# Performance work log

Measured on AMD Instinct MI355X. Metric: run time of the kernel, lower is better.

Reference implementation:

```python
import jax, jax.numpy as jnp
import numpy as np

N_NODES = 100000
EPS = 1e-5


def gcn_conv(x, edge_index, W, b):
    # PyG GCNConv: add self loops, symmetric normalization, aggregate at target.
    n = x.shape[0]
    xw = x @ W                                  # [N, F_out]
    loop = jnp.arange(n)
    src = jnp.concatenate([edge_index[0], loop])
    dst = jnp.concatenate([edge_index[1], loop])
    deg = jax.ops.segment_sum(jnp.ones_like(dst, dtype=xw.dtype), dst, num_segments=n)
    dinv = jnp.where(deg > 0, jax.lax.rsqrt(deg), 0.0)
    norm = dinv[src] * dinv[dst]                # [E+N]
    out = jax.ops.segment_sum(norm[:, None] * xw[src], dst, num_segments=n)
    return out + b


def batch_norm(x, gamma, beta):
    # training-mode BatchNorm1d over node dim
    m = x.mean(axis=0)
    v = x.var(axis=0)
    return (x - m) * jax.lax.rsqrt(v + EPS) * gamma + beta


def setup_inputs() -> dict:
    key = jax.random.key(0)
    ks = jax.random.split(key, 16)
    dims = [(128, 256), (256, 128), (128, 64)]
    inp = {
        "x": jax.random.normal(ks[0], (N_NODES, 128), dtype=jnp.float32),
        "edge_index": jax.random.randint(ks[1], (2, 1600000), 0, N_NODES),
        "pos_edge_index": jax.random.randint(ks[2], (2, 200000), 0, N_NODES),
        "neg_edge_index": jax.random.randint(ks[3], (2, 200000), 0, N_NODES),
    }
    for i, (fi, fo) in enumerate(dims, start=1):
        inp[f"W{i}"] = jax.random.normal(ks[3 + i], (fi, fo), dtype=jnp.float32) / np.sqrt(fi)
        inp[f"b{i}"] = jnp.zeros((fo,), dtype=jnp.float32)
        inp[f"g{i}"] = jnp.ones((fo,), dtype=jnp.float32)
        inp[f"beta{i}"] = jnp.zeros((fo,), dtype=jnp.float32)
    return inp


def reference(x, edge_index, pos_edge_index, neg_edge_index,
              W1, b1, g1, beta1, W2, b2, g2, beta2, W3, b3, g3, beta3):
    # encode
    h = gcn_conv(x, edge_index, W1, b1)
    h = jax.nn.sigmoid(batch_norm(h, g1, beta1))
    h = gcn_conv(h, edge_index, W2, b2)
    h = jax.nn.sigmoid(batch_norm(h, g2, beta2))
    h = gcn_conv(h, edge_index, W3, b3)
    z = batch_norm(h, g3, beta3)                # [N, 64]
    # decode
    ei = jnp.concatenate([pos_edge_index, neg_edge_index], axis=-1)
    logits = jnp.sum(z[ei[0]] * z[ei[1]], axis=-1)
    return logits
```

## Files before the change

### kernel.cpp

```cpp
#include <hip/hip_runtime.h>
#include <hip/hip_bf16.h>
#include <stddef.h>


#define WAVE 64
#define BSHIFT 9
#define SCHUNK 4096

typedef __attribute__((ext_vector_type(8))) short short8;
typedef __attribute__((ext_vector_type(4))) float f32x4;

__device__ __forceinline__ float bl(uint g) { return __uint_as_float(g << 16); }
__device__ __forceinline__ float bh(uint g) { return __uint_as_float(g & 0xffff0000u); }
__device__ __forceinline__ ushort f2b(float f) {
    uint u = __float_as_uint(f);
    return (ushort)((u + 0x7fffu + ((u >> 16) & 1u)) >> 16);
}
__device__ __forceinline__ uint pack2(float lo, float hi) {
    return (uint)f2b(lo) | ((uint)f2b(hi) << 16);
}

__device__ __forceinline__ void gload16(const ushort* g, ushort* l) {
    __builtin_amdgcn_global_load_lds(
        (const __attribute__((address_space(1))) uint*)g,
        (__attribute__((address_space(3))) uint*)l, 16, 0, 0);
}

__global__ __launch_bounds__(256) void k_bhist(const int* __restrict__ dst, int* __restrict__ gh, int E) {
    __shared__ int lh[256];
    lh[threadIdx.x] = 0; __syncthreads();
    int i = blockIdx.x * 256 + threadIdx.x, stride = gridDim.x * 256;
    for (; i < E; i += stride) atomicAdd(&lh[dst[i] >> BSHIFT], 1);
    __syncthreads();
    int v = lh[threadIdx.x];
    if (v) atomicAdd(&gh[threadIdx.x], v);
}

__global__ void k_bscan(const int* __restrict__ gh, int* __restrict__ boff, int* __restrict__ bcur) {
    __shared__ int ls[256];
    int t = threadIdx.x;
    int v = gh[t];
    ls[t] = v; __syncthreads();
    for (int off = 1; off < 256; off <<= 1) {
        int x = (t >= off) ? ls[t - off] : 0;
        __syncthreads();
        ls[t] += x;
        __syncthreads();
    }
    int excl = ls[t] - v;
    boff[t] = excl; bcur[t] = excl;
    if (t == 255) boff[256] = ls[255];
}

__global__ __launch_bounds__(256) void k_bscatter(const int* __restrict__ src, const int* __restrict__ dst,
                                                  int* __restrict__ gcur, uint* __restrict__ pairs, int E) {
    __shared__ int lh[256];
    int t = threadIdx.x;
    int base = blockIdx.x * SCHUNK;
    lh[t] = 0; __syncthreads();
    int rs[16], rd[16];
    #pragma unroll
    for (int i = 0; i < 16; ++i) {
        int idx = base + i * 256 + t;
        if (idx < E) { rs[i] = src[idx]; rd[i] = dst[idx]; atomicAdd(&lh[rd[i] >> BSHIFT], 1); }
        else rd[i] = -1;
    }
    __syncthreads();
    int cnt_b = lh[t];
    int b0 = cnt_b ? atomicAdd(&gcur[t], cnt_b) : 0;
    lh[t] = b0;
    __syncthreads();
    #pragma unroll
    for (int i = 0; i < 16; ++i) {
        if (rd[i] >= 0) {
            int p = atomicAdd(&lh[rd[i] >> BSHIFT], 1);
            pairs[p] = ((uint)(rd[i] & 511) << 17) | (uint)rs[i];
        }
    }
}

__global__ __launch_bounds__(256) void k_bfine(const uint* __restrict__ pairs, const int* __restrict__ boff,
                                               int* __restrict__ rowptr, int* __restrict__ srcs,
                                               float* __restrict__ dinv, int N, int E) {
    __shared__ int lcnt[512];
    __shared__ int ls[256];
    int b = blockIdx.x, t = threadIdx.x;
    int d0 = b << BSHIFT;
    int e0 = boff[b], e1 = boff[b + 1];
    lcnt[t] = 0; lcnt[t + 256] = 0;
    __syncthreads();
    for (int e = e0 + t; e < e1; e += 256)
        atomicAdd(&lcnt[pairs[e] >> 17], 1);
    __syncthreads();
    int c0 = lcnt[2 * t], c1 = lcnt[2 * t + 1];
    ls[t] = c0 + c1;
    __syncthreads();
    for (int off = 1; off < 256; off <<= 1) {
        int x = (t >= off) ? ls[t - off] : 0;
        __syncthreads();
        ls[t] += x;
        __syncthreads();
    }
    int excl = ls[t] - (c0 + c1);
    int s0 = excl, s1 = excl + c0;
    int d = d0 + 2 * t;
    if (d < N)     { rowptr[d] = e0 + s0;     dinv[d] = rsqrtf((float)(c0 + 1)); }
    if (d + 1 < N) { rowptr[d + 1] = e0 + s1; dinv[d + 1] = rsqrtf((float)(c1 + 1)); }
    if (b == 0 && t == 0) rowptr[N] = E;
    lcnt[2 * t] = s0; lcnt[2 * t + 1] = s1;
    __syncthreads();
    for (int e = e0 + t; e < e1; e += 256) {
        uint p = pairs[e];
        int pos = atomicAdd(&lcnt[p >> 17], 1);
        srcs[e0 + pos] = (int)(p & 0x1FFFFu);
    }
}

__global__ void k_conv(const float* __restrict__ W1, const float* __restrict__ W2,
                       const float* __restrict__ W3, ushort* __restrict__ Wt1,
                       ushort* __restrict__ Wt2, ushort* __restrict__ Wt3,
                       const float* __restrict__ x, const float* __restrict__ dinv,
                       ushort* __restrict__ xs, size_t n4) {
    size_t i = (size_t)blockIdx.x * 256 + threadIdx.x;
    if (i < 73728) {
        const float* W; ushort* Wt; int K, Nn; size_t j;
        if (i < 32768)      { W = W1; Wt = Wt1; K = 128; Nn = 256; j = i; }
        else if (i < 65536) { W = W2; Wt = Wt2; K = 256; Nn = 128; j = i - 32768; }
        else                { W = W3; Wt = Wt3; K = 128; Nn = 64;  j = i - 65536; }
        int k = (int)(j / Nn), n = (int)(j % Nn);
        Wt[(size_t)n * K + k] = f2b(W[(size_t)k * Nn + n]);
        return;
    }
    size_t j = i - 73728;
    if (j >= n4) return;
    float d = dinv[j / 32];
    float4 v = reinterpret_cast<const float4*>(x)[j];
    uint2 o;
    o.x = pack2(d * v.x, d * v.y);
    o.y = pack2(d * v.z, d * v.w);
    reinterpret_cast<uint2*>(xs)[j] = o;
}

template<int F, bool STATS>
__global__ __launch_bounds__(256) void k_agg(const ushort* __restrict__ in, ushort* __restrict__ out,
                                             const int* __restrict__ rowptr, const int* __restrict__ srcs,
                                             const float* __restrict__ dinv, int N,
                                             float* __restrict__ gsum, float* __restrict__ gsq) {
    constexpr int L = (F * 2) / 16;
    int wv = threadIdx.x >> 6, lane = threadIdx.x & 63;
    int node = (blockIdx.x * 4 + wv) * (64 / L) + lane / L;
    int sl = lane % L;
    bool act = node < N;
    const uint4* inq = reinterpret_cast<const uint4*>(in);
    float o[8] = {0.f, 0.f, 0.f, 0.f, 0.f, 0.f, 0.f, 0.f};
    if (act) {
        float di = dinv[node];
        float acc[8];
        {
            uint4 v = inq[(size_t)node * L + sl];
            acc[0] = bl(v.x); acc[1] = bh(v.x);
            acc[2] = bl(v.y); acc[3] = bh(v.y);
            acc[4] = bl(v.z); acc[5] = bh(v.z);
            acc[6] = bl(v.w); acc[7] = bh(v.w);
        }
        int e = rowptr[node], e1 = rowptr[node + 1];
        for (; e + 7 < e1; e += 8) {
            int s[8];
            #pragma unroll
            for (int i = 0; i < 8; ++i) s[i] = srcs[e + i];
            uint4 v[8];
            #pragma unroll
            for (int i = 0; i < 8; ++i) v[i] = inq[(size_t)s[i] * L + sl];
            #pragma unroll
            for (int i = 0; i < 8; ++i) {
                acc[0] += bl(v[i].x); acc[1] += bh(v[i].x);
                acc[2] += bl(v[i].y); acc[3] += bh(v[i].y);
                acc[4] += bl(v[i].z); acc[5] += bh(v[i].z);
                acc[6] += bl(v[i].w); acc[7] += bh(v[i].w);
            }
        }
        for (; e + 3 < e1; e += 4) {
            int s[4];
            #pragma unroll
            for (int i = 0; i < 4; ++i) s[i] = srcs[e + i];
            uint4 v[4];
            #pragma unroll
            for (int i = 0; i < 4; ++i) v[i] = inq[(size_t)s[i] * L + sl];
            #pragma unroll
            for (int i = 0; i < 4; ++i) {
                acc[0] += bl(v[i].x); acc[1] += bh(v[i].x);
                acc[2] += bl(v[i].y); acc[3] += bh(v[i].y);
                acc[4] += bl(v[i].z); acc[5] += bh(v[i].z);
                acc[6] += bl(v[i].w); acc[7] += bh(v[i].w);
            }
        }
        for (; e < e1; ++e) {
            uint4 v0 = inq[(size_t)srcs[e] * L + sl];
            acc[0] += bl(v0.x); acc[1] += bh(v0.x);
            acc[2] += bl(v0.y); acc[3] += bh(v0.y);
            acc[4] += bl(v0.z); acc[5] += bh(v0.z);
            acc[6] += bl(v0.w); acc[7] += bh(v0.w);
        }
        #pragma unroll
        for (int j = 0; j < 8; ++j) o[j] = acc[j] * di;
        uint4 ov;
        ov.x = pack2(o[0], o[1]); ov.y = pack2(o[2], o[3]);
        ov.z = pack2(o[4], o[5]); ov.w = pack2(o[6], o[7]);
        reinterpret_cast<uint4*>(out)[(size_t)node * L + sl] = ov;
    }
    if constexpr (STATS) {
        __shared__ float lsum[4][L][8], lsq[4][L][8];
        float s[8], q[8];
        #pragma unroll
        for (int j = 0; j < 8; ++j) { s[j] = o[j]; q[j] = o[j] * o[j]; }
        #pragma unroll
        for (int m = L; m < 64; m <<= 1) {
            #pragma unroll
            for (int j = 0; j < 8; ++j) { s[j] += __shfl_xor(s[j], m); q[j] += __shfl_xor(q[j], m); }
        }
        if (lane < L) {
            #pragma unroll
            for (int j = 0; j < 8; ++j) { lsum[wv][lane][j] = s[j]; lsq[wv][lane][j] = q[j]; }
        }
        __syncthreads();
        int t = threadIdx.x;
        if (t < F) {
            int ch = t / 8, j = t % 8;
            float S = 0.f, Q = 0.f;
            #pragma unroll
            for (int w = 0; w < 4; ++w) { S += lsum[w][ch][j]; Q += lsq[w][ch][j]; }
            atomicAdd(&gsum[t], S); atomicAdd(&gsq[t], Q);
        }
    }
}

template<int K, int NF, int NPASS, bool STATS, bool PRESCALE, bool APPLY>
__global__ __launch_bounds__(256) void k_gemm(const ushort* __restrict__ A, const ushort* __restrict__ Wt,
                                              ushort* __restrict__ C, int M, int Nout,
                                              const float* __restrict__ dinv,
                                              float* __restrict__ gsum, float* __restrict__ gsq,
                                              const float* __restrict__ bsum, const float* __restrict__ bsq,
                                              const float* __restrict__ bg, const float* __restrict__ bb,
                                              float invN) {
    constexpr int S = K / 64;
    constexpr int KS = K / 32;
    __shared__ ushort Alds[2][128 * 64];
    int m0 = blockIdx.x * 128;
    int t = threadIdx.x;
    int w = t >> 6, lane = t & 63;
    int wr = w >> 1, wc = w & 1;
    int rf = lane & 15, kg = lane >> 4;

    auto stage = [&](int buf, int step) {
        #pragma unroll
        for (int i = 0; i < 4; ++i) {
            int cb = (i * 4 + w) * 64;
            int chunk = cb + lane;
            int r = chunk >> 3, cs = chunk & 7;
            int c = cs ^ (r & 7);
            int gr = m0 + r; if (gr >= M) gr = M - 1;
            gload16(A + (size_t)gr * K + step * 64 + c * 8, &Alds[buf][cb * 8]);
        }
    };

    int cg_ = (t & 7) ^ ((t >> 3) & 7);
    auto stageA = [&](int buf, int s) {
        float sc[8], sh[8];
        int fb = s * 64 + cg_ * 8;
        #pragma unroll
        for (int j = 0; j < 8; ++j) {
            float m = bsum[fb + j] * invN;
            float var = bsq[fb + j] * invN - m * m;
            float sv = bg[fb + j] * rsqrtf(var + 1e-5f);
            sc[j] = sv; sh[j] = bb[fb + j] - m * sv;
        }
        #pragma unroll
        for (int i = 0; i < 4; ++i) {
            int r = (t >> 3) + i * 32;
            int gr = m0 + r; if (gr >= M) gr = M - 1;
            uint4 v = *reinterpret_cast<const uint4*>(A + (size_t)gr * K + s * 64 + cg_ * 8);
            uint u[4] = {v.x, v.y, v.z, v.w};
            #pragma unroll
            for (int j = 0; j < 4; ++j) {
                float x0 = bl(u[j]) * sc[2 * j] + sh[2 * j];
                float x1 = bh(u[j]) * sc[2 * j + 1] + sh[2 * j + 1];
                x0 = 1.f / (1.f + __expf(-x0));
                x1 = 1.f / (1.f + __expf(-x1));
                u[j] = pack2(x0, x1);
            }
            v.x = u[0]; v.y = u[1]; v.z = u[2]; v.w = u[3];
            *reinterpret_cast<uint4*>(&Alds[buf][(size_t)(r * 8 + (t & 7)) * 8]) = v;
        }
    };

    auto do_stage = [&](int buf, int step) {
        if constexpr (APPLY) stageA(buf, step); else stage(buf, step);
    };

    float dreg[4][4];
    if constexpr (PRESCALE) {
        #pragma unroll
        for (int mf = 0; mf < 4; ++mf)
            #pragma unroll
            for (int j = 0; j < 4; ++j) {
                int row = m0 + wr * 64 + mf * 16 + kg * 4 + j;
                dreg[mf][j] = (row < M) ? dinv[row] : 0.f;
            }
    }

    for (int pass = 0; pass < NPASS; ++pass) {
        int n0 = pass * NF * 32;
        const ushort* bp[NF];
        #pragma unroll
        for (int nf = 0; nf < NF; ++nf)
            bp[nf] = Wt + (size_t)(n0 + wc * (NF * 16) + nf * 16 + rf) * K + kg * 8;

        f32x4 acc[4][NF];
        #pragma unroll
        for (int mf = 0; mf < 4; ++mf)
            #pragma unroll
            for (int nf = 0; nf < NF; ++nf)
                acc[mf][nf] = (f32x4){0.f, 0.f, 0.f, 0.f};

        if (pass == 0) {
            do_stage(0, 0);
            if constexpr (S == 2) do_stage(1, 1);
            __syncthreads();
        }

        short8 bcur[NF];
        #pragma unroll
        for (int nf = 0; nf < NF; ++nf)
            bcur[nf] = *reinterpret_cast<const short8*>(bp[nf]);

        for (int s = 0; s < S; ++s) {
            if constexpr (S > 2) {
                if (s + 1 < S && pass == 0) do_stage((s + 1) & 1, s + 1);
            }
            #pragma unroll
            for (int ksl = 0; ksl < 2; ++ksl) {
                int gs = s * 2 + ksl;
                short8 bnxt[NF];
                if (gs + 1 < KS) {
                    #pragma unroll
                    for (int nf = 0; nf < NF; ++nf)
                        bnxt[nf] = *reinterpret_cast<const short8*>(bp[nf] + (gs + 1) * 32);
                }
                short8 a[4];
                #pragma unroll
                for (int mf = 0; mf < 4; ++mf) {
                    int R = wr * 64 + mf * 16 + rf;
                    int idx = R * 8 + ((ksl * 4 + kg) ^ (R & 7));
                    a[mf] = *reinterpret_cast<const short8*>(&Alds[s & 1][idx * 8]);
                }
                #pragma unroll
                for (int mf = 0; mf < 4; ++mf)
                    #pragma unroll
                    for (int nf = 0; nf < NF; ++nf)
                        acc[mf][nf] = __builtin_amdgcn_mfma_f32_16x16x32_bf16(a[mf], bcur[nf], acc[mf][nf], 0, 0, 0);
                if (gs + 1 < KS) {
                    #pragma unroll
                    for (int nf = 0; nf < NF; ++nf) bcur[nf] = bnxt[nf];
                }
            }
            if constexpr (S > 2) __syncthreads();
        }

        #pragma unroll
        for (int mf = 0; mf < 4; ++mf)
            #pragma unroll
            for (int nf = 0; nf < NF; ++nf) {
                int col = n0 + wc * (NF * 16) + nf * 16 + rf;
                #pragma unroll
                for (int j = 0; j < 4; ++j) {
                    int row = m0 + wr * 64 + mf * 16 + kg * 4 + j;
                    float v = acc[mf][nf][j];
                    if constexpr (PRESCALE) v *= dreg[mf][j];
                    if (row < M) C[(size_t)row * Nout + col] = f2b(v);
                }
            }

        if constexpr (STATS) {
            __shared__ float bns[2][NF * 32], bnq[2][NF * 32];
            __syncthreads();
            #pragma unroll
            for (int nf = 0; nf < NF; ++nf) {
                float cs = 0.f, cq = 0.f;
                #pragma unroll
                for (int mf = 0; mf < 4; ++mf)
                    #pragma unroll
                    for (int j = 0; j < 4; ++j) {
                        int row = m0 + wr * 64 + mf * 16 + kg * 4 + j;
                        float v = (row < M) ? acc[mf][nf][j] : 0.f;
                        cs += v; cq += v * v;
                    }
                cs += __shfl_xor(cs, 16); cs += __shfl_xor(cs, 32);
                cq += __shfl_xor(cq, 16); cq += __shfl_xor(cq, 32);
                if (kg == 0) { bns[wr][wc * (NF * 16) + nf * 16 + rf] = cs; bnq[wr][wc * (NF * 16) + nf * 16 + rf] = cq; }
            }
            __syncthreads();
            if (t < NF * 32) {
                atomicAdd(&gsum[n0 + t], bns[0][t] + bns[1][t]);
                atomicAdd(&gsq[n0 + t],  bnq[0][t] + bnq[1][t]);
            }
        }
    }
}

__global__ __launch_bounds__(256) void k_decode(const ushort* __restrict__ h,
                                                const float* __restrict__ bsum, const float* __restrict__ bsq,
                                                const float* __restrict__ bg, const float* __restrict__ bb,
                                                float invN,
                                                const int* __restrict__ pos, const int* __restrict__ neg,
                                                int Pp, int Pn, float* __restrict__ out) {
    __shared__ float scl[64], shl[64];
    int t = threadIdx.x;
    if (t < 64) {
        float m = bsum[t] * invN;
        float var = bsq[t] * invN - m * m;
        float sc = bg[t] * rsqrtf(var + 1e-5f);
        scl[t] = sc; shl[t] = bb[t] - m * sc;
    }
    __syncthreads();
    int gid = blockIdx.x * 16 + (t >> 4);
    int l = t & 15;
    int P = Pp + Pn;
    if (gid >= P) return;
    int a, b;
    if (gid < Pp) { a = pos[gid]; b = pos[Pp + gid]; }
    else          { int e = gid - Pp; a = neg[e]; b = neg[Pn + e]; }
    const uint2* hu = reinterpret_cast<const uint2*>(h);
    uint2 ua = hu[(size_t)a * 16 + l];
    uint2 ub = hu[(size_t)b * 16 + l];
    int f = l * 4;
    float s0 = scl[f], s1 = scl[f + 1], s2 = scl[f + 2], s3 = scl[f + 3];
    float t0 = shl[f], t1 = shl[f + 1], t2 = shl[f + 2], t3 = shl[f + 3];
    float a0 = bl(ua.x) * s0 + t0, a1 = bh(ua.x) * s1 + t1, a2 = bl(ua.y) * s2 + t2, a3 = bh(ua.y) * s3 + t3;
    float b0 = bl(ub.x) * s0 + t0, b1 = bh(ub.x) * s1 + t1, b2 = bl(ub.y) * s2 + t2, b3 = bh(ub.y) * s3 + t3;
    float d = a0 * b0 + a1 * b1 + a2 * b2 + a3 * b3;
    d += __shfl_xor(d, 1);
    d += __shfl_xor(d, 2);
    d += __shfl_xor(d, 4);
    d += __shfl_xor(d, 8);
    if (l == 0) out[gid] = d;
}

extern "C" void kernel_launch(void* const* d_in, const int* in_sizes, int n_in,
                              void* d_out, int out_size, void* d_ws, size_t ws_size,
                              hipStream_t stream) {
    const float* x   = (const float*)d_in[0];
    const int*   ei  = (const int*)d_in[1];
    const int*   pe  = (const int*)d_in[2];
    const int*   ne  = (const int*)d_in[3];
    const float* W1  = (const float*)d_in[4];
    const float* g1  = (const float*)d_in[6];
    const float* be1 = (const float*)d_in[7];
    const float* W2  = (const float*)d_in[8];
    const float* g2  = (const float*)d_in[10];
    const float* be2 = (const float*)d_in[11];
    const float* W3  = (const float*)d_in[12];
    const float* g3  = (const float*)d_in[14];
    const float* be3 = (const float*)d_in[15];
    float* out = (float*)d_out;

    const int N  = in_sizes[0] / 128;
    const int E  = in_sizes[1] / 2;
    const int Pp = in_sizes[2] / 2;
    const int Pn = in_sizes[3] / 2;
    const float invN = 1.0f / (float)N;

    char* ws = (char*)d_ws;
    auto carve = [&](size_t bytes) -> char* {
        char* p = ws;
        ws += (bytes + 255) & ~(size_t)255;
        return p;
    };
    char*  zz     = carve(256 * 4 + 896 * 4);
    int*   gh     = (int*)zz;
    float* sums1  = (float*)(zz + 1024);
    float* sq1    = sums1 + 256;
    float* sums2  = sq1 + 256;
    float* sq2    = sums2 + 128;
    float* sums3  = sq2 + 128;
    float* sq3    = sums3 + 64;
    size_t zz_bytes = 1024 + 896 * 4;

    int*    boff   = (int*)carve(257 * 4);
    int*    bcur   = (int*)carve(256 * 4);
    int*    rowptr = (int*)carve((size_t)(N + 1) * 4);
    float*  dinv   = (float*)carve((size_t)N * 4);
    int*    srcs   = (int*)carve((size_t)E * 4);
    uint*   pairs  = (uint*)carve((size_t)E * 4);
    ushort* Wt1    = (ushort*)carve(128 * 256 * 2);
    ushort* Wt2    = (ushort*)carve(256 * 128 * 2);
    ushort* Wt3    = (ushort*)carve(128 * 64 * 2);
    ushort* b1     = (ushort*)carve((size_t)N * 128 * 2);
    ushort* b2     = (ushort*)carve((size_t)N * 128 * 2);
    ushort* b3     = (ushort*)carve((size_t)N * 256 * 2);

    const int* e_src = ei;
    const int* e_dst = ei + E;
    const int NBUCK = (N + (1 << BSHIFT) - 1) >> BSHIFT;

    hipMemsetAsync(zz, 0, zz_bytes, stream);

    k_bhist<<<2048, 256, 0, stream>>>(e_dst, gh, E);
    k_bscan<<<1, 256, 0, stream>>>(gh, boff, bcur);
    k_bscatter<<<(E + SCHUNK - 1) / SCHUNK, 256, 0, stream>>>(e_src, e_dst, bcur, pairs, E);
    k_bfine<<<NBUCK, 256, 0, stream>>>(pairs, boff, rowptr, srcs, dinv, N, E);

    {
        size_t n4 = (size_t)N * 128 / 4;
        int blocks = (int)((73728 + n4 + 255) / 256);
        k_conv<<<blocks, 256, 0, stream>>>(W1, W2, W3, Wt1, Wt2, Wt3, x, dinv, b1, n4);
    }

    const int mblk = (N + 127) / 128;
    const int agg128 = (N + 15) / 16;
    const int agg64  = (N + 31) / 32;

    k_agg<128, false><<<agg128, 256, 0, stream>>>(b1, b2, rowptr, srcs, dinv, N, nullptr, nullptr);
    k_gemm<128, 4, 2, true, false, false><<<mblk, 256, 0, stream>>>(
        b2, Wt1, b3, N, 256, nullptr, sums1, sq1, nullptr, nullptr, nullptr, nullptr, invN);

    k_gemm<256, 4, 1, false, true, true><<<mblk, 256, 0, stream>>>(
        b3, Wt2, b1, N, 128, dinv, nullptr, nullptr, sums1, sq1, g1, be1, invN);
    k_agg<128, true><<<agg128, 256, 0, stream>>>(b1, b2, rowptr, srcs, dinv, N, sums2, sq2);

    k_gemm<128, 2, 1, false, true, true><<<mblk, 256, 0, stream>>>(
        b2, Wt3, b1, N, 64, dinv, nullptr, nullptr, sums2, sq2, g2, be2, invN);
    k_agg<64, true><<<agg64, 256, 0, stream>>>(b1, b2, rowptr, srcs, dinv, N, sums3, sq3);

    k_decode<<<(Pp + Pn + 15) / 16, 256, 0, stream>>>(b2, sums3, sq3, g3, be3, invN,
                                                      pe, ne, Pp, Pn, out);
}
```

Before: 658.0 us.

## Merge preprocessing kernels, drop dinv prescale of x, split BN stats from aggregation

Fuses the destination histogram, weight transpose/convert, and x-to-bf16 conversion into one launch, so the x conversion no longer waits on the CSR build for dinv. The first aggregation now applies the source dinv per edge through an extra gather. BatchNorm statistics move out of the aggregation kernels into a separate grid-strided reduction kernel, which removes the shared-memory reduction and atomics from the aggregation. In exchange it adds launches, re-reads the aggregated output, and the first layer performs per-edge dinv gathers.

```diff
diff --git a/kernel.cpp b/kernel.cpp
--- a/kernel.cpp
+++ b/kernel.cpp
@@ -6,6 +6,9 @@
 #define WAVE 64
 #define BSHIFT 9
 #define SCHUNK 4096
+#define HB 2048
+#define WB 288
+#define XB 2048
 
 typedef __attribute__((ext_vector_type(8))) short short8;
 typedef __attribute__((ext_vector_type(4))) float f32x4;
@@ -26,14 +29,37 @@
         (__attribute__((address_space(3))) uint*)l, 16, 0, 0);
 }
 
-__global__ __launch_bounds__(256) void k_bhist(const int* __restrict__ dst, int* __restrict__ gh, int E) {
-    __shared__ int lh[256];
-    lh[threadIdx.x] = 0; __syncthreads();
-    int i = blockIdx.x * 256 + threadIdx.x, stride = gridDim.x * 256;
-    for (; i < E; i += stride) atomicAdd(&lh[dst[i] >> BSHIFT], 1);
-    __syncthreads();
-    int v = lh[threadIdx.x];
-    if (v) atomicAdd(&gh[threadIdx.x], v);
+__global__ __launch_bounds__(256) void k_pre(const int* __restrict__ dst, int* __restrict__ gh, int E,
+                                             const float* __restrict__ W1, const float* __restrict__ W2,
+                                             const float* __restrict__ W3, ushort* __restrict__ Wt1,
+                                             ushort* __restrict__ Wt2, ushort* __restrict__ Wt3,
+                                             const float* __restrict__ x, ushort* __restrict__ xb,
+                                             size_t nx2) {
+    int b = blockIdx.x, t = threadIdx.x;
+    if (b < HB) {
+        __shared__ int lh[256];
+        lh[t] = 0; __syncthreads();
+        for (int i = b * 256 + t; i < E; i += HB * 256) atomicAdd(&lh[dst[i] >> BSHIFT], 1);
+        __syncthreads();
+        int v = lh[t];
+        if (v) atomicAdd(&gh[t], v);
+    } else if (b < HB + WB) {
+        int i = (b - HB) * 256 + t;
+        const float* W; ushort* Wt; int K, Nn, j;
+        if (i < 32768)      { W = W1; Wt = Wt1; K = 128; Nn = 256; j = i; }
+        else if (i < 65536) { W = W2; Wt = Wt2; K = 256; Nn = 128; j = i - 32768; }
+        else                { W = W3; Wt = Wt3; K = 128; Nn = 64;  j = i - 65536; }
+        int k = j / Nn, n = j % Nn;
+        Wt[(size_t)n * K + k] = f2b(W[(size_t)k * Nn + n]);
+    } else {
+        for (size_t i = (size_t)(b - HB - WB) * 256 + t; i < nx2; i += (size_t)XB * 256) {
+            float4 v = reinterpret_cast<const float4*>(x)[i];
+            uint2 o;
+            o.x = pack2(v.x, v.y);
+            o.y = pack2(v.z, v.w);
+            reinterpret_cast<uint2*>(xb)[i] = o;
+        }
+    }
 }
 
 __global__ void k_bscan(const int* __restrict__ gh, int* __restrict__ boff, int* __restrict__ bcur) {
@@ -116,121 +142,106 @@
     }
 }
 
-__global__ void k_conv(const float* __restrict__ W1, const float* __restrict__ W2,
-                       const float* __restrict__ W3, ushort* __restrict__ Wt1,
-                       ushort* __restrict__ Wt2, ushort* __restrict__ Wt3,
-                       const float* __restrict__ x, const float* __restrict__ dinv,
-                       ushort* __restrict__ xs, size_t n4) {
-    size_t i = (size_t)blockIdx.x * 256 + threadIdx.x;
-    if (i < 73728) {
-        const float* W; ushort* Wt; int K, Nn; size_t j;
-        if (i < 32768)      { W = W1; Wt = Wt1; K = 128; Nn = 256; j = i; }
-        else if (i < 65536) { W = W2; Wt = Wt2; K = 256; Nn = 128; j = i - 32768; }
-        else                { W = W3; Wt = Wt3; K = 128; Nn = 64;  j = i - 65536; }
-        int k = (int)(j / Nn), n = (int)(j % Nn);
-        Wt[(size_t)n * K + k] = f2b(W[(size_t)k * Nn + n]);
-        return;
-    }
-    size_t j = i - 73728;
-    if (j >= n4) return;
-    float d = dinv[j / 32];
-    float4 v = reinterpret_cast<const float4*>(x)[j];
-    uint2 o;
-    o.x = pack2(d * v.x, d * v.y);
-    o.y = pack2(d * v.z, d * v.w);
-    reinterpret_cast<uint2*>(xs)[j] = o;
-}
-
-template<int F, bool STATS>
+template<int F, bool SIN>
 __global__ __launch_bounds__(256) void k_agg(const ushort* __restrict__ in, ushort* __restrict__ out,
                                              const int* __restrict__ rowptr, const int* __restrict__ srcs,
-                                             const float* __restrict__ dinv, int N,
-                                             float* __restrict__ gsum, float* __restrict__ gsq) {
+                                             const float* __restrict__ dinv, int N) {
     constexpr int L = (F * 2) / 16;
     int wv = threadIdx.x >> 6, lane = threadIdx.x & 63;
     int node = (blockIdx.x * 4 + wv) * (64 / L) + lane / L;
     int sl = lane % L;
-    bool act = node < N;
+    if (node >= N) return;
     const uint4* inq = reinterpret_cast<const uint4*>(in);
-    float o[8] = {0.f, 0.f, 0.f, 0.f, 0.f, 0.f, 0.f, 0.f};
-    if (act) {
-        float di = dinv[node];
-        float acc[8];
-        {
-            uint4 v = inq[(size_t)node * L + sl];
-            acc[0] = bl(v.x); acc[1] = bh(v.x);
-            acc[2] = bl(v.y); acc[3] = bh(v.y);
-            acc[4] = bl(v.z); acc[5] = bh(v.z);
-            acc[6] = bl(v.w); acc[7] = bh(v.w);
-        }
-        int e = rowptr[node], e1 = rowptr[node + 1];
-        for (; e + 7 < e1; e += 8) {
-            int s[8];
-            #pragma unroll
-            for (int i = 0; i < 8; ++i) s[i] = srcs[e + i];
-            uint4 v[8];
-            #pragma unroll
-            for (int i = 0; i < 8; ++i) v[i] = inq[(size_t)s[i] * L + sl];
-            #pragma unroll
-            for (int i = 0; i < 8; ++i) {
-                acc[0] += bl(v[i].x); acc[1] += bh(v[i].x);
-                acc[2] += bl(v[i].y); acc[3] += bh(v[i].y);
-                acc[4] += bl(v[i].z); acc[5] += bh(v[i].z);
-                acc[6] += bl(v[i].w); acc[7] += bh(v[i].w);
-            }
-        }
-        for (; e + 3 < e1; e += 4) {
-            int s[4];
-            #pragma unroll
-            for (int i = 0; i < 4; ++i) s[i] = srcs[e + i];
-            uint4 v[4];
-            #pragma unroll
-            for (int i = 0; i < 4; ++i) v[i] = inq[(size_t)s[i] * L + sl];
-            #pragma unroll
-            for (int i = 0; i < 4; ++i) {
-                acc[0] += bl(v[i].x); acc[1] += bh(v[i].x);
-                acc[2] += bl(v[i].y); acc[3] += bh(v[i].y);
-                acc[4] += bl(v[i].z); acc[5] += bh(v[i].z);
-                acc[6] += bl(v[i].w); acc[7] += bh(v[i].w);
-            }
-        }
-        for (; e < e1; ++e) {
-            uint4 v0 = inq[(size_t)srcs[e] * L + sl];
-            acc[0] += bl(v0.x); acc[1] += bh(v0.x);
-            acc[2] += bl(v0.y); acc[3] += bh(v0.y);
-            acc[4] += bl(v0.z); acc[5] += bh(v0.z);
-            acc[6] += bl(v0.w); acc[7] += bh(v0.w);
-        }
-        #pragma unroll
-        for (int j = 0; j < 8; ++j) o[j] = acc[j] * di;
-        uint4 ov;
-        ov.x = pack2(o[0], o[1]); ov.y = pack2(o[2], o[3]);
-        ov.z = pack2(o[4], o[5]); ov.w = pack2(o[6], o[7]);
-        reinterpret_cast<uint4*>(out)[(size_t)node * L + sl] = ov;
-    }
-    if constexpr (STATS) {
-        __shared__ float lsum[4][L][8], lsq[4][L][8];
-        float s[8], q[8];
-        #pragma unroll
-        for (int j = 0; j < 8; ++j) { s[j] = o[j]; q[j] = o[j] * o[j]; }
-        #pragma unroll
-        for (int m = L; m < 64; m <<= 1) {
-            #pragma unroll
-            for (int j = 0; j < 8; ++j) { s[j] += __shfl_xor(s[j], m); q[j] += __shfl_xor(q[j], m); }
-        }
-        if (lane < L) {
-            #pragma unroll
-            for (int j = 0; j < 8; ++j) { lsum[wv][lane][j] = s[j]; lsq[wv][lane][j] = q[j]; }
-        }
-        __syncthreads();
-        int t = threadIdx.x;
-        if (t < F) {
-            int ch = t / 8, j = t % 8;
-            float S = 0.f, Q = 0.f;
-            #pragma unroll
-            for (int w = 0; w < 4; ++w) { S += lsum[w][ch][j]; Q += lsq[w][ch][j]; }
-            atomicAdd(&gsum[t], S); atomicAdd(&gsq[t], Q);
-        }
+    float di = dinv[node];
+    float acc[8];
+    {
+        uint4 v = inq[(size_t)node * L + sl];
+        float sf = SIN ? 1.f : di;
+        acc[0] = sf * bl(v.x); acc[1] = sf * bh(v.x);
+        acc[2] = sf * bl(v.y); acc[3] = sf * bh(v.y);
+        acc[4] = sf * bl(v.z); acc[5] = sf * bh(v.z);
+        acc[6] = sf * bl(v.w); acc[7] = sf * bh(v.w);
+    }
+    int e = rowptr[node], e1 = rowptr[node + 1];
+    for (; e + 7 < e1; e += 8) {
+        int s[8];
+        #pragma unroll
+        for (int i = 0; i < 8; ++i) s[i] = srcs[e + i];
+        float dd[8];
+        if constexpr (!SIN) {
+            #pragma unroll
+            for (int i = 0; i < 8; ++i) dd[i] = dinv[s[i]];
+        }
+        uint4 v[8];
+        #pragma unroll
+        for (int i = 0; i < 8; ++i) v[i] = inq[(size_t)s[i] * L + sl];
+        #pragma unroll
+        for (int i = 0; i < 8; ++i) {
+            float d0 = SIN ? 1.f : dd[i];
+            acc[0] += d0 * bl(v[i].x); acc[1] += d0 * bh(v[i].x);
+            acc[2] += d0 * bl(v[i].y); acc[3] += d0 * bh(v[i].y);
+            acc[4] += d0 * bl(v[i].z); acc[5] += d0 * bh(v[i].z);
+            acc[6] += d0 * bl(v[i].w); acc[7] += d0 * bh(v[i].w);
+        }
+    }
+    for (; e < e1; ++e) {
+        int s0 = srcs[e];
+        float d0 = SIN ? 1.f : dinv[s0];
+        uint4 v0 = inq[(size_t)s0 * L + sl];
+        acc[0] += d0 * bl(v0.x); acc[1] += d0 * bh(v0.x);
+        acc[2] += d0 * bl(v0.y); acc[3] += d0 * bh(v0.y);
+        acc[4] += d0 * bl(v0.z); acc[5] += d0 * bh(v0.z);
+        acc[6] += d0 * bl(v0.w); acc[7] += d0 * bh(v0.w);
+    }
+    uint4 o;
+    o.x = pack2(acc[0] * di, acc[1] * di);
+    o.y = pack2(acc[2] * di, acc[3] * di);
+    o.z = pack2(acc[4] * di, acc[5] * di);
+    o.w = pack2(acc[6] * di, acc[7] * di);
+    reinterpret_cast<uint4*>(out)[(size_t)node * L + sl] = o;
+}
+
+template<int F>
+__global__ __launch_bounds__(256) void k_bnstats(const ushort* __restrict__ h, float* __restrict__ gsum,
+                                                 float* __restrict__ gsq, int N) {
+    constexpr int C = F / 8;
+    constexpr int RPW = 64 / C;
+    __shared__ float ls[4][16][16];
+    int wv = threadIdx.x >> 6, lane = threadIdx.x & 63;
+    int fidx = lane % C, rsub = lane / C;
+    int row = (blockIdx.x * 4 + wv) * RPW + rsub;
+    int rstride = gridDim.x * 4 * RPW;
+    const uint4* hq = reinterpret_cast<const uint4*>(h);
+    float s[8] = {}, q[8] = {};
+    for (int r = row; r < N; r += rstride) {
+        uint4 v = hq[(size_t)r * C + fidx];
+        float x;
+        x = bl(v.x); s[0] += x; q[0] += x * x;
+        x = bh(v.x); s[1] += x; q[1] += x * x;
+        x = bl(v.y); s[2] += x; q[2] += x * x;
+        x = bh(v.y); s[3] += x; q[3] += x * x;
+        x = bl(v.z); s[4] += x; q[4] += x * x;
+        x = bh(v.z); s[5] += x; q[5] += x * x;
+        x = bl(v.w); s[6] += x; q[6] += x * x;
+        x = bh(v.w); s[7] += x; q[7] += x * x;
+    }
+    #pragma unroll
+    for (int m = C; m < 64; m <<= 1) {
+        #pragma unroll
+        for (int j = 0; j < 8; ++j) { s[j] += __shfl_xor(s[j], m); q[j] += __shfl_xor(q[j], m); }
+    }
+    if (lane < C) {
+        #pragma unroll
+        for (int j = 0; j < 8; ++j) { ls[wv][lane][j] = s[j]; ls[wv][lane][8 + j] = q[j]; }
+    }
+    __syncthreads();
+    int t = threadIdx.x;
+    if (t < F) {
+        int ch = t / 8, j = t % 8;
+        float S = 0.f, Q = 0.f;
+        #pragma unroll
+        for (int w = 0; w < 4; ++w) { S += ls[w][ch][j]; Q += ls[w][ch][8 + j]; }
+        atomicAdd(&gsum[t], S); atomicAdd(&gsq[t], Q);
     }
 }
 
@@ -504,32 +515,32 @@
 
     hipMemsetAsync(zz, 0, zz_bytes, stream);
 
-    k_bhist<<<2048, 256, 0, stream>>>(e_dst, gh, E);
+    {
+        size_t nx2 = (size_t)N * 128 / 4;
+        k_pre<<<HB + WB + XB, 256, 0, stream>>>(e_dst, gh, E, W1, W2, W3, Wt1, Wt2, Wt3,
+                                                x, b1, nx2);
+    }
     k_bscan<<<1, 256, 0, stream>>>(gh, boff, bcur);
     k_bscatter<<<(E + SCHUNK - 1) / SCHUNK, 256, 0, stream>>>(e_src, e_dst, bcur, pairs, E);
     k_bfine<<<NBUCK, 256, 0, stream>>>(pairs, boff, rowptr, srcs, dinv, N, E);
 
-    {
-        size_t n4 = (size_t)N * 128 / 4;
-        int blocks = (int)((73728 + n4 + 255) / 256);
-        k_conv<<<blocks, 256, 0, stream>>>(W1, W2, W3, Wt1, Wt2, Wt3, x, dinv, b1, n4);
-    }
-
     const int mblk = (N + 127) / 128;
     const int agg128 = (N + 15) / 16;
     const int agg64  = (N + 31) / 32;
 
-    k_agg<128, false><<<agg128, 256, 0, stream>>>(b1, b2, rowptr, srcs, dinv, N, nullptr, nullptr);
+    k_agg<128, false><<<agg128, 256, 0, stream>>>(b1, b2, rowptr, srcs, dinv, N);
     k_gemm<128, 4, 2, true, false, false><<<mblk, 256, 0, stream>>>(
         b2, Wt1, b3, N, 256, nullptr, sums1, sq1, nullptr, nullptr, nullptr, nullptr, invN);
 
     k_gemm<256, 4, 1, false, true, true><<<mblk, 256, 0, stream>>>(
         b3, Wt2, b1, N, 128, dinv, nullptr, nullptr, sums1, sq1, g1, be1, invN);
-    k_agg<128, true><<<agg128, 256, 0, stream>>>(b1, b2, rowptr, srcs, dinv, N, sums2, sq2);
+    k_agg<128, true><<<agg128, 256, 0, stream>>>(b1, b2, rowptr, srcs, dinv, N);
+    k_bnstats<128><<<512, 256, 0, stream>>>(b2, sums2, sq2, N);
 
     k_gemm<128, 2, 1, false, true, true><<<mblk, 256, 0, stream>>>(
         b2, Wt3, b1, N, 64, dinv, nullptr, nullptr, sums2, sq2, g2, be2, invN);
-    k_agg<64, true><<<agg64, 256, 0, stream>>>(b1, b2, rowptr, srcs, dinv, N, sums3, sq3);
+    k_agg<64, true><<<agg64, 256, 0, stream>>>(b1, b2, rowptr, srcs, dinv, N);
+    k_bnstats<64><<<512, 256, 0, stream>>>(b2, sums3, sq3, N);
 
     k_decode<<<(Pp + Pn + 15) / 16, 256, 0, stream>>>(b2, sums3, sq3, g3, be3, invN,
                                                       pe, ne, Pp, Pn, out);
```

Result: faster. 541.9 us (-17.7%).
